# Optimization experiments

Measured on AMD Instinct MI355X. Metric: run time of the kernel, lower is better.

## Reference

```python
import jax, jax.numpy as jnp
import numpy as np

KS = 3          # kernel_size
DIL = 6         # dilation
PAD = 6         # padding
N = KS * KS     # sampling points per pixel
EPS = 1e-5      # BatchNorm eps


def conv2d(x, w, b=None, padding=0):
    out = jax.lax.conv_general_dilated(
        x, w, window_strides=(1, 1),
        padding=[(padding, padding), (padding, padding)],
        dimension_numbers=('NCHW', 'OIHW', 'NCHW'))
    if b is not None:
        out = out + b[None, :, None, None]
    return out


def setup_inputs() -> dict:
    key = jax.random.key(0)
    ks = jax.random.split(key, 6)
    B, C, H, W, P = 4, 256, 64, 64, 256
    x = jax.random.normal(ks[0], (B, C, H, W), jnp.float32)
    # offset-predicting conv (2N channels), kaiming-ish scale, kept small so offsets are sane
    w_p = jax.random.normal(ks[1], (2 * N, C, 3, 3), jnp.float32) * 0.02
    b_p = jnp.zeros((2 * N,), jnp.float32)
    # modulation-mask conv (N channels)
    w_m = jax.random.normal(ks[2], (N, C, 3, 3), jnp.float32) * 0.02
    b_m = jnp.zeros((N,), jnp.float32)
    # main deform-conv weight (no bias)
    w = jax.random.normal(ks[3], (P, C, KS, KS), jnp.float32) * (2.0 / (C * N)) ** 0.5
    gamma = jnp.ones((P,), jnp.float32)   # BN weight (init fill 1)
    beta = jnp.zeros((P,), jnp.float32)   # BN bias  (init fill 0)
    return dict(x=x, w_p=w_p, b_p=b_p, w_m=w_m, b_m=b_m, w=w, gamma=gamma, beta=beta)


def deform_conv(x, w_p, b_p, w_m, b_m, w):
    B, C, H, W = x.shape
    offset = conv2d(x, w_p, b_p, padding=1)                 # [B, 2N, H, W]
    m = jax.nn.sigmoid(conv2d(x, w_m, b_m, padding=1))      # [B, N, H, W] modulation mask

    x_pad = jnp.pad(x, ((0, 0), (0, 0), (PAD, PAD), (PAD, PAD)))
    Hp, Wp = H + 2 * PAD, W + 2 * PAD

    # p = p_0 (base grid, starts at 1 into padded map) + p_n (dilated kernel grid) + offset
    r = (KS - 1) // 2
    pn = jnp.arange(-r, r + 1, dtype=jnp.float32) * DIL
    pn_x, pn_y = jnp.meshgrid(pn, pn, indexing='ij')        # row-major matches conv weight layout
    p0_x = jnp.arange(1, H + 1, dtype=jnp.float32)
    p0_y = jnp.arange(1, W + 1, dtype=jnp.float32)
    off_x = offset[:, :N].transpose(0, 2, 3, 1)             # [B, H, W, N]
    off_y = offset[:, N:].transpose(0, 2, 3, 1)
    px = p0_x[None, :, None, None] + pn_x.reshape(-1)[None, None, None, :] + off_x
    py = p0_y[None, None, :, None] + pn_y.reshape(-1)[None, None, None, :] + off_y

    q_lt_x = jnp.clip(jnp.floor(px), 0, Hp - 1)
    q_lt_y = jnp.clip(jnp.floor(py), 0, Wp - 1)
    q_rb_x = jnp.clip(jnp.floor(px) + 1, 0, Hp - 1)
    q_rb_y = jnp.clip(jnp.floor(py) + 1, 0, Wp - 1)
    px = jnp.clip(px, 0, Hp - 1)
    py = jnp.clip(py, 0, Wp - 1)

    x_flat = x_pad.reshape(B, C, Hp * Wp)

    def gather(qx, qy):
        idx = (qx * Wp + qy).astype(jnp.int32).reshape(B, 1, -1)   # [B,1,H*W*N]
        v = jnp.take_along_axis(x_flat, jnp.broadcast_to(idx, (B, C, idx.shape[-1])), axis=2)
        return v.reshape(B, C, H, W, N)

    # bilinear weights (deform-conv-v2 formulation)
    g_lt = (1 + (q_lt_x - px)) * (1 + (q_lt_y - py))
    g_rb = (1 - (q_rb_x - px)) * (1 - (q_rb_y - py))
    g_lb = (1 + (q_lt_x - px)) * (1 - (q_rb_y - py))
    g_rt = (1 - (q_rb_x - px)) * (1 + (q_lt_y - py))

    x_off = (g_lt[:, None] * gather(q_lt_x, q_lt_y)
             + g_rb[:, None] * gather(q_rb_x, q_rb_y)
             + g_lb[:, None] * gather(q_lt_x, q_rb_y)
             + g_rt[:, None] * gather(q_rb_x, q_lt_y))     # [B, C, H, W, N]

    x_off = x_off * m.transpose(0, 2, 3, 1)[:, None]        # apply modulation

    # stride-KS conv over the tiled x_offset == einsum over kernel positions
    wk = w.reshape(w.shape[0], C, N)
    return jnp.einsum('bchwk,ock->bohw', x_off, wk)


def reference(x, w_p, b_p, w_m, b_m, w, gamma, beta):
    y = deform_conv(x, w_p, b_p, w_m, b_m, w)
    # BatchNorm2d, training mode (batch stats, biased variance)
    mean = y.mean(axis=(0, 2, 3), keepdims=True)
    var = ((y - mean) ** 2).mean(axis=(0, 2, 3), keepdims=True)
    y = (y - mean) * jax.lax.rsqrt(var + EPS)
    y = y * gamma[None, :, None, None] + beta[None, :, None, None]
    return jax.nn.relu(y)
```

## Files before the change

kernel.cpp:

```cpp
#include <hip/hip_runtime.h>
#include <math.h>

#define CC 256
#define PP 256
#define XSTR 296

#define WS_OFF   0ull
#define WS_Y     442368ull
#define WS_SUM   4636672ull
#define WS_SUMSQ 4636928ull
#define WS_SCALE 4637184ull
#define WS_SHIFT 4637440ull
#define WS_XT    4637696ull
#define WS_WF    8832000ull
#define WS_WPMF  9126912ull

typedef __attribute__((ext_vector_type(8))) short bf16x8;
typedef __attribute__((ext_vector_type(4))) float f32x4;

static __device__ inline unsigned short f2bf(float f) {
  unsigned int u = __float_as_uint(f);
  unsigned int r = (u + 0x7FFFu + ((u >> 16) & 1u)) >> 16;
  return (unsigned short)r;
}

__global__ __launch_bounds__(256) void k_prep(const float* __restrict__ x,
                                              const float* __restrict__ w,
                                              const float* __restrict__ w_p,
                                              const float* __restrict__ w_m,
                                              float* __restrict__ ws) {
  int blk = blockIdx.x, t = threadIdx.x;
  if (blk < 1024) {
    __shared__ float sT[64][65];
    int b = blk >> 8, h = (blk >> 2) & 63, c0 = (blk & 3) * 64;
    const float* xs = x + ((size_t)(b * 256 + c0) * 64 + h) * 64;
    int cl = t >> 6, wl = t & 63;
#pragma unroll
    for (int it = 0; it < 16; ++it) {
      int c = cl + it * 4;
      sT[c][wl] = xs[(size_t)c * 4096 + wl];
    }
    __syncthreads();
    float* xt = ws + WS_XT + ((size_t)b * 64 + h) * 16384 + c0;
    int c2 = t & 63, w2l = t >> 6;
#pragma unroll
    for (int it = 0; it < 16; ++it) {
      int w2 = w2l + it * 4;
      xt[(size_t)w2 * 256 + c2] = sT[c2][w2];
    }
  } else {
    int gid = (blk - 1024) * 256 + t;
    if (blk == 1024 && t < 512) ws[WS_SUM + t] = 0.f;
    unsigned short* wfb = (unsigned short*)(ws + WS_WF);
    for (int e = gid; e < 589824; e += 163840) {
      int j = e & 7, ocin = (e >> 3) & 15, quad = (e >> 7) & 3;
      int ot = (e >> 9) & 15, ksg = e >> 13;
      int kb = ksg / 9, ks = ksg - kb * 9;
      int c = kb * 32 + quad * 8 + j;
      int oc = ot * 16 + ocin;
      wfb[e] = f2bf(w[((size_t)oc * CC + c) * 9 + ks]);
    }
    unsigned short* wpmf = (unsigned short*)(ws + WS_WPMF);
    for (int e = gid; e < 73728; e += 163840) {
      int j = e & 7, ocin = (e >> 3) & 15, quad = (e >> 7) & 3;
      int ot = (e >> 9) & 1, ksg = e >> 10;
      int kb = ksg / 9, ks = ksg - kb * 9;
      int c = kb * 32 + quad * 8 + j;
      int oc = ot * 16 + ocin;
      float v = 0.f;
      if (oc < 18)      v = w_p[((size_t)oc * CC + c) * 9 + ks];
      else if (oc < 27) v = w_m[((size_t)(oc - 18) * CC + c) * 9 + ks];
      wpmf[e] = f2bf(v);
    }
  }
}

__global__ __launch_bounds__(512, 4) void k_offmask(const float* __restrict__ b_p,
                                                    const float* __restrict__ b_m,
                                                    float* __restrict__ ws) {
  const float* xT = ws + WS_XT;
  const unsigned short* wpmf = (const unsigned short*)(ws + WS_WPMF);
  float* offm = ws + WS_OFF;
  __shared__ __align__(16) unsigned short sXo[32 * XSTR];

  int t = threadIdx.x, blk = blockIdx.x;
  int xcd = blk & 7, ii = blk >> 3;
  int b = xcd >> 1, h = (xcd & 1) * 32 + (ii >> 1), side = ii & 1;

  int lane = t & 63, wv = __builtin_amdgcn_readfirstlane(t >> 6);
  int pxt = wv & 1, ot = (wv >> 1) & 1, kh = wv >> 2;
  f32x4 acc = {0.f, 0.f, 0.f, 0.f};
  const float4* xb4 = (const float4*)(xT + (size_t)b * 1048576);
  const unsigned short* bb =
      &sXo[(pxt * 16 + (lane & 15)) * XSTR + (lane >> 4) * 8];
  int uq = t >> 3, q = t & 7;

  for (int kb = 0; kb < 8; ++kb) {
    __syncthreads();
#pragma unroll
    for (int r = 0; r < 5; ++r) {
      int u = r * 64 + uq;
      if (u < 288) {
        int j = u >> 5, px = u & 31;
        int row = h + j / 3 - 1, col = side * 32 + px + j % 3 - 1;
        float4 v = {0.f, 0.f, 0.f, 0.f};
        if ((unsigned)row < 64u && (unsigned)col < 64u)
          v = xb4[(row * 64 + col) * 64 + kb * 8 + q];
        unsigned p0 = (unsigned)f2bf(v.x) | ((unsigned)f2bf(v.y) << 16);
        unsigned p1 = (unsigned)f2bf(v.z) | ((unsigned)f2bf(v.w) << 16);
        *(uint2*)&sXo[px * XSTR + j * 32 + q * 4] = (uint2){p0, p1};
      }
    }
    __syncthreads();
#pragma unroll
    for (int ks = 0; ks < 9; ++ks) {
      if ((int)(ks >= 5) == kh) {
        int ksg = kb * 9 + ks;
        bf16x8 af =
            *(const bf16x8*)(wpmf + (size_t)ksg * 1024 + ot * 512 + lane * 8);
        bf16x8 bf = *(const bf16x8*)(bb + ks * 32);
        acc = __builtin_amdgcn_mfma_f32_16x16x32_bf16(af, bf, acc, 0, 0, 0);
      }
    }
  }
  __syncthreads();
  float* sR = (float*)sXo;
  if (kh == 1) {
    int base = (pxt * 2 + ot) * 256 + lane * 4;
#pragma unroll
    for (int r = 0; r < 4; ++r) sR[base + r] = acc[r];
  }
  __syncthreads();
  if (kh == 0) {
    int base = (pxt * 2 + ot) * 256 + lane * 4;
    int pxl = side * 32 + pxt * 16 + (lane & 15);
#pragma unroll
    for (int r = 0; r < 4; ++r) {
      int oc = ot * 16 + (lane >> 4) * 4 + r;
      if (oc < 27) {
        float v = acc[r] + sR[base + r];
        v += (oc < 18) ? b_p[oc] : b_m[oc - 18];
        if (oc >= 18) v = 1.f / (1.f + expf(-v));
        offm[((size_t)b * 27 + oc) * 4096 + h * 64 + pxl] = v;
      }
    }
  }
}

__global__ __launch_bounds__(512, 4) void k_deform(float* __restrict__ ws) {
  const float* offm = ws + WS_OFF;
  const float* xT = ws + WS_XT;
  const unsigned short* wfb = (const unsigned short*)(ws + WS_WF);
  float* y = ws + WS_Y;

  __shared__ __align__(16) uint4 sPK[288];
  __shared__ __align__(16) unsigned short sXu[32 * XSTR];

  int t = threadIdx.x, blk = blockIdx.x;
  int xcd = blk & 7, ii = blk >> 3;
  int b = xcd >> 1, h = (xcd & 1) * 32 + (ii >> 1), side = ii & 1;

  if (t < 288) {
    int k = t >> 5, w = side * 32 + (t & 31);
    size_t base = ((size_t)b * 27) * 4096 + h * 64 + w;
    float offx = offm[base + (size_t)k * 4096];
    float offy = offm[base + (size_t)(9 + k) * 4096];
    float mk   = offm[base + (size_t)(18 + k) * 4096];
    float pnx = (float)((k / 3 - 1) * 6);
    float pny = (float)((k % 3 - 1) * 6);
    float pxf = (float)(h + 1) + pnx + offx;
    float pyf = (float)(w + 1) + pny + offy;
    float fx = floorf(pxf), fy = floorf(pyf);
    float q0x = fminf(fmaxf(fx, 0.f), 75.f);
    float q1x = fminf(fmaxf(fx + 1.f, 0.f), 75.f);
    float q0y = fminf(fmaxf(fy, 0.f), 75.f);
    float q1y = fminf(fmaxf(fy + 1.f, 0.f), 75.f);
    float pxc = fminf(fmaxf(pxf, 0.f), 75.f);
    float pyc = fminf(fmaxf(pyf, 0.f), 75.f);
    float glt = (1.f + (q0x - pxc)) * (1.f + (q0y - pyc));
    float grb = (1.f - (q1x - pxc)) * (1.f - (q1y - pyc));
    float glb = (1.f + (q0x - pxc)) * (1.f - (q1y - pyc));
    float grt = (1.f - (q1x - pxc)) * (1.f + (q0y - pyc));
    int ix0 = (int)q0x - 6, ix1 = (int)q1x - 6;
    int iy0 = (int)q0y - 6, iy1 = (int)q1y - 6;
    bool v00 = (unsigned)ix0 < 64u && (unsigned)iy0 < 64u;
    bool v11 = (unsigned)ix1 < 64u && (unsigned)iy1 < 64u;
    bool v01 = (unsigned)ix0 < 64u && (unsigned)iy1 < 64u;
    bool v10 = (unsigned)ix1 < 64u && (unsigned)iy0 < 64u;
    unsigned a0 = v00 ? (unsigned)(ix0 * 64 + iy0) : 0u;
    unsigned a1 = v11 ? (unsigned)(ix1 * 64 + iy1) : 0u;
    unsigned a2 = v01 ? (unsigned)(ix0 * 64 + iy1) : 0u;
    unsigned a3 = v10 ? (unsigned)(ix1 * 64 + iy0) : 0u;
    float g0 = v00 ? glt * mk : 0.f;
    float g1 = v11 ? grb * mk : 0.f;
    float g2 = v01 ? glb * mk : 0.f;
    float g3 = v10 ? grt * mk : 0.f;
    uint4 pk;
    pk.x = a0 | (a1 << 16);
    pk.y = a2 | (a3 << 16);
    pk.z = (unsigned)f2bf(g0) | ((unsigned)f2bf(g1) << 16);
    pk.w = (unsigned)f2bf(g2) | ((unsigned)f2bf(g3) << 16);
    sPK[t] = pk;
  }

  int lane = t & 63, wv = __builtin_amdgcn_readfirstlane(t >> 6);
  f32x4 acc[2][2];
#pragma unroll
  for (int i = 0; i < 2; ++i)
#pragma unroll
    for (int jj = 0; jj < 2; ++jj) acc[i][jj] = (f32x4){0.f, 0.f, 0.f, 0.f};

  const float4* xb4 = (const float4*)(xT + (size_t)b * 1048576);
  const unsigned short* bb0 = &sXu[(lane & 15) * XSTR + (lane >> 4) * 8];
  const unsigned short* bb1 = bb0 + 16 * XSTR;
  int uq = t >> 3, q = t & 7;

  for (int kb = 0; kb < 8; ++kb) {
    __syncthreads();
#pragma unroll
    for (int r = 0; r < 5; ++r) {
      int u = r * 64 + uq;
      if (u < 288) {
        uint4 pk = sPK[u];
        int k = u >> 5, px = u & 31;
        int cb = kb * 8 + q;
        float4 v0 = xb4[(int)(pk.x & 0xFFFFu) * 64 + cb];
        float4 v1 = xb4[(int)(pk.x >> 16) * 64 + cb];
        float4 v2 = xb4[(int)(pk.y & 0xFFFFu) * 64 + cb];
        float4 v3 = xb4[(int)(pk.y >> 16) * 64 + cb];
        float g0 = __uint_as_float((pk.z & 0xFFFFu) << 16);
        float g1 = __uint_as_float(pk.z & 0xFFFF0000u);
        float g2 = __uint_as_float((pk.w & 0xFFFFu) << 16);
        float g3 = __uint_as_float(pk.w & 0xFFFF0000u);
        float4 val;
        val.x = fmaf(g3, v3.x, fmaf(g2, v2.x, fmaf(g1, v1.x, g0 * v0.x)));
        val.y = fmaf(g3, v3.y, fmaf(g2, v2.y, fmaf(g1, v1.y, g0 * v0.y)));
        val.z = fmaf(g3, v3.z, fmaf(g2, v2.z, fmaf(g1, v1.z, g0 * v0.z)));
        val.w = fmaf(g3, v3.w, fmaf(g2, v2.w, fmaf(g1, v1.w, g0 * v0.w)));
        unsigned p0 = (unsigned)f2bf(val.x) | ((unsigned)f2bf(val.y) << 16);
        unsigned p1 = (unsigned)f2bf(val.z) | ((unsigned)f2bf(val.w) << 16);
        *(uint2*)&sXu[px * XSTR + k * 32 + q * 4] = (uint2){p0, p1};
      }
    }
    __syncthreads();
#pragma unroll
    for (int ks = 0; ks < 9; ++ks) {
      int ksg = kb * 9 + ks;
      const unsigned short* ap =
          wfb + (size_t)ksg * 8192 + (size_t)wv * 1024 + lane * 8;
      bf16x8 af0 = *(const bf16x8*)ap;
      bf16x8 af1 = *(const bf16x8*)(ap + 512);
      bf16x8 bf0 = *(const bf16x8*)(bb0 + ks * 32);
      bf16x8 bf1 = *(const bf16x8*)(bb1 + ks * 32);
      acc[0][0] = __builtin_amdgcn_mfma_f32_16x16x32_bf16(af0, bf0, acc[0][0], 0, 0, 0);
      acc[0][1] = __builtin_amdgcn_mfma_f32_16x16x32_bf16(af0, bf1, acc[0][1], 0, 0, 0);
      acc[1][0] = __builtin_amdgcn_mfma_f32_16x16x32_bf16(af1, bf0, acc[1][0], 0, 0, 0);
      acc[1][1] = __builtin_amdgcn_mfma_f32_16x16x32_bf16(af1, bf1, acc[1][1], 0, 0, 0);
    }
  }

  __syncthreads();
  float* sP = (float*)sXu;
  float* sP2 = sP + 256;
  int quad = lane >> 4, li = lane & 15;
  size_t ybase = ((size_t)b * PP) * 4096 + h * 64 + side * 32;
#pragma unroll
  for (int otl = 0; otl < 2; ++otl) {
#pragma unroll
    for (int r = 0; r < 4; ++r) {
      int oc = wv * 32 + otl * 16 + quad * 4 + r;
      float v0 = acc[otl][0][r];
      float v1 = acc[otl][1][r];
      float* yp = y + ybase + (size_t)oc * 4096 + li;
      yp[0] = v0;
      yp[16] = v1;
      float s = v0 + v1;
      float s2 = fmaf(v0, v0, v1 * v1);
      s += __shfl_xor(s, 1);  s2 += __shfl_xor(s2, 1);
      s += __shfl_xor(s, 2);  s2 += __shfl_xor(s2, 2);
      s += __shfl_xor(s, 4);  s2 += __shfl_xor(s2, 4);
      s += __shfl_xor(s, 8);  s2 += __shfl_xor(s2, 8);
      if (li == 0) {
        sP[oc] = s;
        sP2[oc] = s2;
      }
    }
  }
  __syncthreads();
  if (t < 256) {
    atomicAdd(&ws[WS_SUM + t], sP[t]);
    atomicAdd(&ws[WS_SUMSQ + t], sP2[t]);
  }
}

__global__ void k_stats(float* __restrict__ ws, const float* __restrict__ gamma,
                        const float* __restrict__ beta) {
  int t = threadIdx.x;
  float s  = ws[WS_SUM + t];
  float s2 = ws[WS_SUMSQ + t];
  float mean = s * (1.f / 16384.f);
  float var  = fmaf(s2, 1.f / 16384.f, -mean * mean);
  float rstd = rsqrtf(var + 1e-5f);
  float sc = gamma[t] * rstd;
  ws[WS_SCALE + t] = sc;
  ws[WS_SHIFT + t] = fmaf(-mean, sc, beta[t]);
}

__global__ void k_bnrelu(const float* __restrict__ ws, float* __restrict__ out) {
  const float4* y4 = (const float4*)(ws + WS_Y);
  const float* scale = ws + WS_SCALE;
  const float* shift = ws + WS_SHIFT;
  float4* o4 = (float4*)out;
  const int n4 = 4 * PP * 1024;
  for (int i = blockIdx.x * blockDim.x + threadIdx.x; i < n4;
       i += gridDim.x * blockDim.x) {
    int oc = (i >> 10) & 255;
    float sc = scale[oc], sh = shift[oc];
    float4 v = y4[i];
    float4 r;
    r.x = fmaxf(fmaf(v.x, sc, sh), 0.f);
    r.y = fmaxf(fmaf(v.y, sc, sh), 0.f);
    r.z = fmaxf(fmaf(v.z, sc, sh), 0.f);
    r.w = fmaxf(fmaf(v.w, sc, sh), 0.f);
    o4[i] = r;
  }
}

extern "C" void kernel_launch(void* const* d_in, const int* in_sizes, int n_in,
                              void* d_out, int out_size, void* d_ws,
                              size_t ws_size, hipStream_t stream) {
  const float* x     = (const float*)d_in[0];
  const float* w_p   = (const float*)d_in[1];
  const float* b_p   = (const float*)d_in[2];
  const float* w_m   = (const float*)d_in[3];
  const float* b_m   = (const float*)d_in[4];
  const float* w     = (const float*)d_in[5];
  const float* gamma = (const float*)d_in[6];
  const float* beta  = (const float*)d_in[7];
  float* ws  = (float*)d_ws;
  float* out = (float*)d_out;

  k_prep<<<1664, 256, 0, stream>>>(x, w, w_p, w_m, ws);
  k_offmask<<<512, 512, 0, stream>>>(b_p, b_m, ws);
  k_deform<<<512, 512, 0, stream>>>(ws);
  k_stats<<<1, 256, 0, stream>>>(ws, gamma, beta);
  k_bnrelu<<<2048, 256, 0, stream>>>(ws, out);
}
```

Measured before the change: 169.7 us.

## Double-buffer LDS staging in offset-mask and deform kernels with hoisted gather addresses

Both the offset/mask conv kernel and the deformable conv kernel now use two LDS tiles. Each iteration stages the next channel block while MFMAs consume the current one, which removes one barrier per iteration. Per-thread gather addresses and bilinear weights are computed once into registers instead of being re-read from sPK every channel block. The cost is more LDS per block, which may lower occupancy, and higher register pressure under launch_bounds(512,4), which could cause spills.

```diff
diff --git a/kernel.cpp b/kernel.cpp
--- a/kernel.cpp
+++ b/kernel.cpp
@@ -81,7 +81,8 @@
   const float* xT = ws + WS_XT;
   const unsigned short* wpmf = (const unsigned short*)(ws + WS_WPMF);
   float* offm = ws + WS_OFF;
-  __shared__ __align__(16) unsigned short sXo[32 * XSTR];
+  __shared__ __align__(16) unsigned short sXo0[32 * XSTR];
+  __shared__ __align__(16) unsigned short sXo1[32 * XSTR];
 
   int t = threadIdx.x, blk = blockIdx.x;
   int xcd = blk & 7, ii = blk >> 3;
@@ -91,27 +92,46 @@
   int pxt = wv & 1, ot = (wv >> 1) & 1, kh = wv >> 2;
   f32x4 acc = {0.f, 0.f, 0.f, 0.f};
   const float4* xb4 = (const float4*)(xT + (size_t)b * 1048576);
-  const unsigned short* bb =
-      &sXo[(pxt * 16 + (lane & 15)) * XSTR + (lane >> 4) * 8];
   int uq = t >> 3, q = t & 7;
 
-  for (int kb = 0; kb < 8; ++kb) {
-    __syncthreads();
+  int oa[5], odst[5];
+#pragma unroll
+  for (int r = 0; r < 5; ++r) {
+    int u = r * 64 + uq;
+    if (u < 288) {
+      int j = u >> 5, px = u & 31;
+      int row = h + j / 3 - 1, col = side * 32 + px + j % 3 - 1;
+      odst[r] = px * XSTR + j * 32 + q * 4;
+      oa[r] = ((unsigned)row < 64u && (unsigned)col < 64u)
+                  ? (row * 64 + col) * 64 + q : -1;
+    } else {
+      odst[r] = -1;
+      oa[r] = -1;
+    }
+  }
+
+  auto stage = [&](int kb, unsigned short* buf) {
+    int cb = kb * 8;
 #pragma unroll
     for (int r = 0; r < 5; ++r) {
-      int u = r * 64 + uq;
-      if (u < 288) {
-        int j = u >> 5, px = u & 31;
-        int row = h + j / 3 - 1, col = side * 32 + px + j % 3 - 1;
+      if (odst[r] >= 0) {
         float4 v = {0.f, 0.f, 0.f, 0.f};
-        if ((unsigned)row < 64u && (unsigned)col < 64u)
-          v = xb4[(row * 64 + col) * 64 + kb * 8 + q];
+        if (oa[r] >= 0) v = xb4[oa[r] + cb];
         unsigned p0 = (unsigned)f2bf(v.x) | ((unsigned)f2bf(v.y) << 16);
         unsigned p1 = (unsigned)f2bf(v.z) | ((unsigned)f2bf(v.w) << 16);
-        *(uint2*)&sXo[px * XSTR + j * 32 + q * 4] = (uint2){p0, p1};
-      }
-    }
-    __syncthreads();
+        *(uint2*)&buf[odst[r]] = (uint2){p0, p1};
+      }
+    }
+  };
+
+  stage(0, sXo0);
+  __syncthreads();
+  for (int kb = 0; kb < 8; ++kb) {
+    unsigned short* cur = (kb & 1) ? sXo1 : sXo0;
+    unsigned short* nxt = (kb & 1) ? sXo0 : sXo1;
+    if (kb < 7) stage(kb + 1, nxt);
+    const unsigned short* bb =
+        &cur[(pxt * 16 + (lane & 15)) * XSTR + (lane >> 4) * 8];
 #pragma unroll
     for (int ks = 0; ks < 9; ++ks) {
       if ((int)(ks >= 5) == kh) {
@@ -122,9 +142,10 @@
         acc = __builtin_amdgcn_mfma_f32_16x16x32_bf16(af, bf, acc, 0, 0, 0);
       }
     }
-  }
-  __syncthreads();
-  float* sR = (float*)sXo;
+    __syncthreads();
+  }
+
+  float* sR = (float*)sXo0;
   if (kh == 1) {
     int base = (pxt * 2 + ot) * 256 + lane * 4;
 #pragma unroll
@@ -154,7 +175,8 @@
   float* y = ws + WS_Y;
 
   __shared__ __align__(16) uint4 sPK[288];
-  __shared__ __align__(16) unsigned short sXu[32 * XSTR];
+  __shared__ __align__(16) unsigned short sXu0[32 * XSTR];
+  __shared__ __align__(16) unsigned short sXu1[32 * XSTR];
 
   int t = threadIdx.x, blk = blockIdx.x;
   int xcd = blk & 7, ii = blk >> 3;
@@ -202,6 +224,30 @@
     pk.w = (unsigned)f2bf(g2) | ((unsigned)f2bf(g3) << 16);
     sPK[t] = pk;
   }
+  __syncthreads();
+
+  int uq = t >> 3, q = t & 7;
+  int ta0[5], ta1[5], ta2[5], ta3[5], tdst[5];
+  float tg0[5], tg1[5], tg2[5], tg3[5];
+#pragma unroll
+  for (int r = 0; r < 5; ++r) {
+    int u = r * 64 + uq;
+    if (u < 288) {
+      uint4 pk = sPK[u];
+      int k = u >> 5, px = u & 31;
+      ta0[r] = (int)(pk.x & 0xFFFFu) * 64 + q;
+      ta1[r] = (int)(pk.x >> 16) * 64 + q;
+      ta2[r] = (int)(pk.y & 0xFFFFu) * 64 + q;
+      ta3[r] = (int)(pk.y >> 16) * 64 + q;
+      tg0[r] = __uint_as_float((pk.z & 0xFFFFu) << 16);
+      tg1[r] = __uint_as_float(pk.z & 0xFFFF0000u);
+      tg2[r] = __uint_as_float((pk.w & 0xFFFFu) << 16);
+      tg3[r] = __uint_as_float(pk.w & 0xFFFF0000u);
+      tdst[r] = px * XSTR + k * 32 + q * 4;
+    } else {
+      tdst[r] = -1;
+    }
+  }
 
   int lane = t & 63, wv = __builtin_amdgcn_readfirstlane(t >> 6);
   f32x4 acc[2][2];
@@ -211,27 +257,17 @@
     for (int jj = 0; jj < 2; ++jj) acc[i][jj] = (f32x4){0.f, 0.f, 0.f, 0.f};
 
   const float4* xb4 = (const float4*)(xT + (size_t)b * 1048576);
-  const unsigned short* bb0 = &sXu[(lane & 15) * XSTR + (lane >> 4) * 8];
-  const unsigned short* bb1 = bb0 + 16 * XSTR;
-  int uq = t >> 3, q = t & 7;
-
-  for (int kb = 0; kb < 8; ++kb) {
-    __syncthreads();
+
+  auto stage = [&](int kb, unsigned short* buf) {
+    int cb = kb * 8;
 #pragma unroll
     for (int r = 0; r < 5; ++r) {
-      int u = r * 64 + uq;
-      if (u < 288) {
-        uint4 pk = sPK[u];
-        int k = u >> 5, px = u & 31;
-        int cb = kb * 8 + q;
-        float4 v0 = xb4[(int)(pk.x & 0xFFFFu) * 64 + cb];
-        float4 v1 = xb4[(int)(pk.x >> 16) * 64 + cb];
-        float4 v2 = xb4[(int)(pk.y & 0xFFFFu) * 64 + cb];
-        float4 v3 = xb4[(int)(pk.y >> 16) * 64 + cb];
-        float g0 = __uint_as_float((pk.z & 0xFFFFu) << 16);
-        float g1 = __uint_as_float(pk.z & 0xFFFF0000u);
-        float g2 = __uint_as_float((pk.w & 0xFFFFu) << 16);
-        float g3 = __uint_as_float(pk.w & 0xFFFF0000u);
+      if (tdst[r] >= 0) {
+        float4 v0 = xb4[ta0[r] + cb];
+        float4 v1 = xb4[ta1[r] + cb];
+        float4 v2 = xb4[ta2[r] + cb];
+        float4 v3 = xb4[ta3[r] + cb];
+        float g0 = tg0[r], g1 = tg1[r], g2 = tg2[r], g3 = tg3[r];
         float4 val;
         val.x = fmaf(g3, v3.x, fmaf(g2, v2.x, fmaf(g1, v1.x, g0 * v0.x)));
         val.y = fmaf(g3, v3.y, fmaf(g2, v2.y, fmaf(g1, v1.y, g0 * v0.y)));
@@ -239,10 +275,19 @@
         val.w = fmaf(g3, v3.w, fmaf(g2, v2.w, fmaf(g1, v1.w, g0 * v0.w)));
         unsigned p0 = (unsigned)f2bf(val.x) | ((unsigned)f2bf(val.y) << 16);
         unsigned p1 = (unsigned)f2bf(val.z) | ((unsigned)f2bf(val.w) << 16);
-        *(uint2*)&sXu[px * XSTR + k * 32 + q * 4] = (uint2){p0, p1};
-      }
-    }
-    __syncthreads();
+        *(uint2*)&buf[tdst[r]] = (uint2){p0, p1};
+      }
+    }
+  };
+
+  stage(0, sXu0);
+  __syncthreads();
+  for (int kb = 0; kb < 8; ++kb) {
+    unsigned short* cur = (kb & 1) ? sXu1 : sXu0;
+    unsigned short* nxt = (kb & 1) ? sXu0 : sXu1;
+    if (kb < 7) stage(kb + 1, nxt);
+    const unsigned short* bb0 = &cur[(lane & 15) * XSTR + (lane >> 4) * 8];
+    const unsigned short* bb1 = bb0 + 16 * XSTR;
 #pragma unroll
     for (int ks = 0; ks < 9; ++ks) {
       int ksg = kb * 9 + ks;
@@ -257,10 +302,10 @@
       acc[1][0] = __builtin_amdgcn_mfma_f32_16x16x32_bf16(af1, bf0, acc[1][0], 0, 0, 0);
       acc[1][1] = __builtin_amdgcn_mfma_f32_16x16x32_bf16(af1, bf1, acc[1][1], 0, 0, 0);
     }
-  }
-
-  __syncthreads();
-  float* sP = (float*)sXu;
+    __syncthreads();
+  }
+
+  float* sP = (float*)sPK;
   float* sP2 = sP + 256;
   int quad = lane >> 4, li = lane & 15;
   size_t ybase = ((size_t)b * PP) * 4096 + h * 64 + side * 32;
```

After: 167.9 us. Within noise of the previous version (-1.1%).
